# Kernel optimization log

Measured on AMD Instinct MI355X. Metric: run time of the kernel, lower is better.

## Reference

```python
import jax, jax.numpy as jnp
import numpy as np

DEPTH = 24; D_MODEL = 192; D_INNER = 384; D_STATE = 16; DT_RANK = 12; D_CONV = 4
H = 32; W = 3200; P = 16; NP = (W // P) * (H // P)  # 400 patches
NCLS = 22; BATCH = 4; EPS = 1e-5


def _rmsnorm(x, w):
    return x * jax.lax.rsqrt(jnp.mean(x * x, axis=-1, keepdims=True) + EPS) * w


def _causal_dwconv(x, w, b):
    # x: (B, L, D), w: (D, K) depthwise, left-padded causal conv (mamba conv1d)
    D = x.shape[-1]; K = w.shape[-1]
    xp = jnp.pad(jnp.swapaxes(x, 1, 2), ((0, 0), (0, 0), (K - 1, 0)))
    y = jax.lax.conv_general_dilated(xp, w[:, None, :], (1,), 'VALID',
            dimension_numbers=('NCH', 'OIH', 'NCH'), feature_group_count=D)
    return jnp.swapaxes(y + b[None, :, None], 1, 2)


def _selective_scan(x, dt, Bm, Cm, A, Dsk):
    # x, dt: (B, L, d); Bm, Cm: (B, L, n); A: (d, n); Dsk: (d,)
    dA = jnp.exp(dt[..., None] * A)                  # (B, L, d, n)
    dBx = (dt * x)[..., None] * Bm[:, :, None, :]    # (B, L, d, n)
    h0 = jnp.zeros((x.shape[0], x.shape[2], A.shape[1]), x.dtype)

    def step(h, inp):
        a, bx, c = inp
        h = a * h + bx
        return h, jnp.einsum('bdn,bn->bd', h, c)

    _, ys = jax.lax.scan(step, h0,
        (jnp.swapaxes(dA, 0, 1), jnp.swapaxes(dBx, 0, 1), jnp.swapaxes(Cm, 0, 1)))
    return jnp.swapaxes(ys, 0, 1) + x * Dsk


def _mamba_dir(xz, cw_l, cb_l, xpw, dtw, dtb, A, Dsk):
    xx, z = jnp.split(xz, 2, axis=-1)
    xx = jax.nn.silu(_causal_dwconv(xx, cw_l, cb_l))
    dbl = xx @ xpw.T                                  # (B, L, dt_rank + 2n)
    dt = jax.nn.softplus(dbl[..., :DT_RANK] @ dtw.T + dtb)
    Bm = dbl[..., DT_RANK:DT_RANK + D_STATE]
    Cm = dbl[..., DT_RANK + D_STATE:]
    y = _selective_scan(xx, dt, Bm, Cm, A, Dsk)
    return y * jax.nn.silu(z)


def _forward(x, pe_w, pe_b, cls_token, pos_embed, norm_w, in_proj_w, cw, cb,
             xproj_w, dtproj_w, dtproj_b, A_log, A_b_log, Dp, outproj_w,
             norm_f_w, head_w, head_b):
    B = x.shape[0]
    # patch embed: conv2d stride=kernel=16 on (B,1,H,W)
    y = jax.lax.conv_general_dilated(x[:, None], pe_w, (P, P), 'VALID',
            dimension_numbers=('NCHW', 'OIHW', 'NCHW')) + pe_b[None, :, None, None]
    tok = jnp.transpose(y, (0, 2, 3, 1)).reshape(B, -1, D_MODEL)   # (B, NP, D)
    tok = jnp.concatenate([jnp.broadcast_to(cls_token, (B, 1, D_MODEL)), tok], axis=1)
    tok = tok + pos_embed

    def layer_step(carry, p):
        hidden, residual = carry
        nw, ipw, cw_l, cb_l, xpw, dtw, dtb, Al, Abl, Dsk, opw = p
        residual = residual + hidden          # fused add (residual_in_fp32: all fp32)
        h = _rmsnorm(residual, nw)
        xz = h @ ipw.T                         # (B, L, 2*d_inner)
        y_f = _mamba_dir(xz, cw_l, cb_l, xpw, dtw, dtb, -jnp.exp(Al), Dsk)
        y_b = _mamba_dir(xz[:, ::-1], cw_l, cb_l, xpw, dtw, dtb, -jnp.exp(Abl), Dsk)[:, ::-1]
        return ((y_f + y_b) @ opw.T, residual), None

    # NOTE: source sets residual = x AND hidden = x before the loop, so the
    (hidden, residual), _ = jax.lax.scan(
        layer_step, (tok, tok),
        (norm_w, in_proj_w, cw, cb, xproj_w, dtproj_w, dtproj_b, A_log, A_b_log, Dp, outproj_w))
    out = _rmsnorm(residual + hidden, norm_f_w)
    return out[:, 0] @ head_w.T + head_b          # (B, n_classes)


def setup_inputs() -> dict:
    key = jax.random.key(0)
    ks = jax.random.split(key, 12)

    def n(k, shape, scale):
        return jax.random.normal(k, shape, jnp.float32) * scale

    a_init = jnp.tile(jnp.log(jnp.arange(1, D_STATE + 1, dtype=jnp.float32))[None, None, :],
                      (DEPTH, D_INNER, 1))
    return {
        'x': n(ks[0], (BATCH, H, W), 1.0),
        'pe_w': n(ks[1], (D_MODEL, 1, P, P), 1.0 / P),
        'pe_b': jnp.zeros((D_MODEL,), jnp.float32),
        'cls_token': n(ks[2], (1, 1, D_MODEL), 0.02),
        'pos_embed': n(ks[3], (1, NP + 1, D_MODEL), 0.02),
        'norm_w': jnp.ones((DEPTH, D_MODEL), jnp.float32),
        'in_proj_w': n(ks[4], (DEPTH, 2 * D_INNER, D_MODEL), D_MODEL ** -0.5),
        'cw': n(ks[5], (DEPTH, D_INNER, D_CONV), D_CONV ** -0.5),
        'cb': jnp.zeros((DEPTH, D_INNER), jnp.float32),
        'xproj_w': n(ks[6], (DEPTH, DT_RANK + 2 * D_STATE, D_INNER), D_INNER ** -0.5),
        'dtproj_w': n(ks[7], (DEPTH, D_INNER, DT_RANK), DT_RANK ** -0.5),
        'dtproj_b': n(ks[8], (DEPTH, D_INNER), 0.1),
        'A_log': a_init,
        'A_b_log': a_init,
        'Dp': jnp.ones((DEPTH, D_INNER), jnp.float32),
        'outproj_w': n(ks[9], (DEPTH, D_MODEL, D_INNER), D_INNER ** -0.5 / np.sqrt(DEPTH)),
        'norm_f_w': jnp.ones((D_MODEL,), jnp.float32),
        'head_w': n(ks[10], (NCLS, D_MODEL), D_MODEL ** -0.5),
        'head_b': jnp.zeros((NCLS,), jnp.float32),
    }


def reference(x, pe_w, pe_b, cls_token, pos_embed, norm_w, in_proj_w, cw, cb,
              xproj_w, dtproj_w, dtproj_b, A_log, A_b_log, Dp, outproj_w,
              norm_f_w, head_w, head_b):
    return _forward(x, pe_w, pe_b, cls_token, pos_embed, norm_w, in_proj_w, cw, cb,
                    xproj_w, dtproj_w, dtproj_b, A_log, A_b_log, Dp, outproj_w,
                    norm_f_w, head_w, head_b)
```

## Files before the change

kernel.cpp:

```cpp
#include <hip/hip_runtime.h>
#include <hip/hip_bf16.h>

#define DEPTH 24
#define DM 192
#define DI 384
#define DS 16
#define DR 12
#define LSEQ 401
#define BATCH 4
#define NTOK (BATCH*LSEQ)
#define NCLS 22
#define NC 16
#define TCH 26

__device__ __forceinline__ float silu_f(float x) { return x / (1.f + __expf(-x)); }

__global__ void patch_embed_k(const float* __restrict__ x,
                              const float* __restrict__ pe_w,
                              const float* __restrict__ pe_b,
                              const float* __restrict__ cls,
                              const float* __restrict__ pos,
                              float* __restrict__ residual, float* __restrict__ hidden)
{
    __shared__ float xp[4][256];
    int g0 = blockIdx.x * 4;
    int c = threadIdx.x;
    #pragma unroll
    for (int j = 0; j < 4; j++) {
        int g = g0 + j;
        int b = g / LSEQ, t = g % LSEQ;
        if (t != 0) {
            int p = t - 1, pi = p / 200, pj = p % 200;
            for (int i = c; i < 256; i += 192) {
                int pp = i >> 4, qq = i & 15;
                xp[j][i] = x[((size_t)(b * 32 + pi * 16 + pp)) * 3200 + pj * 16 + qq];
            }
        }
    }
    __syncthreads();
    float acc[4] = {0.f, 0.f, 0.f, 0.f};
    for (int k = 0; k < 256; k++) {
        float w = pe_w[c * 256 + k];
        #pragma unroll
        for (int j = 0; j < 4; j++) acc[j] += xp[j][k] * w;
    }
    #pragma unroll
    for (int j = 0; j < 4; j++) {
        int g = g0 + j;
        int t = g % LSEQ;
        float v = (t == 0) ? cls[c] : (acc[j] + pe_b[c]);
        v += pos[t * DM + c];
        residual[(size_t)g * DM + c] = v;
        hidden[(size_t)g * DM + c] = v;
    }
}

__global__ __launch_bounds__(192) void prenorm_k(
    const float* __restrict__ resin, float* __restrict__ hidden,
    float* __restrict__ resout, float* __restrict__ hnorm,
    const float* __restrict__ nw, float* __restrict__ dbl)
{
    __shared__ float wsum[3][4];
    int c = threadIdx.x;
    int t0 = blockIdx.x * 4;
    int wave = c >> 6, lane = c & 63;
    float r[4], s[4];
    #pragma unroll
    for (int j = 0; j < 4; j++) {
        int idx = (t0 + j) * DM + c;
        r[j] = resin[idx] + hidden[idx];
        s[j] = r[j] * r[j];
    }
    #pragma unroll
    for (int off = 32; off > 0; off >>= 1) {
        #pragma unroll
        for (int j = 0; j < 4; j++) s[j] += __shfl_down(s[j], off);
    }
    if (lane == 0) {
        #pragma unroll
        for (int j = 0; j < 4; j++) wsum[wave][j] = s[j];
    }
    __syncthreads();
    float nwv = nw[c];
    #pragma unroll
    for (int j = 0; j < 4; j++) {
        float tot = wsum[0][j] + wsum[1][j] + wsum[2][j];
        float rms = rsqrtf(tot / (float)DM + 1e-5f);
        int idx = (t0 + j) * DM + c;
        resout[idx] = r[j];
        hnorm[idx] = r[j] * rms * nwv;
        hidden[idx] = 0.f;
    }
    for (int i = blockIdx.x * 192 + c; i < 2 * NTOK * 44; i += 401 * 192)
        dbl[i] = 0.f;
}

__global__ __launch_bounds__(256) void gemm_xz_k(
    const float* __restrict__ hnorm, const float* __restrict__ ipw,
    float* __restrict__ xz)
{
    constexpr int KS = 48;
    __shared__ float As[KS][68];
    __shared__ float Ws[KS][68];
    int tid = threadIdx.x;
    int bn = blockIdx.x * 64;
    int bm = blockIdx.y * 64;
    int r0 = (tid >> 4) * 4;
    int c0 = (tid & 15) * 4;
    int srow = tid >> 2, sk = (tid & 3) * 12;
    float acc[4][4] = {};
    for (int k0 = 0; k0 < DM; k0 += KS) {
        {
            int m = bm + srow;
            const float* ap = hnorm + (size_t)m * DM + k0 + sk;
            #pragma unroll
            for (int i = 0; i < 12; i++)
                As[sk + i][srow] = (m < NTOK) ? ap[i] : 0.f;
            const float* wp = ipw + (size_t)(bn + srow) * DM + k0 + sk;
            #pragma unroll
            for (int i = 0; i < 12; i++)
                Ws[sk + i][srow] = wp[i];
        }
        __syncthreads();
        #pragma unroll
        for (int kk = 0; kk < KS; kk++) {
            float4 a = *(const float4*)&As[kk][r0];
            float4 w = *(const float4*)&Ws[kk][c0];
            acc[0][0] += a.x * w.x; acc[0][1] += a.x * w.y; acc[0][2] += a.x * w.z; acc[0][3] += a.x * w.w;
            acc[1][0] += a.y * w.x; acc[1][1] += a.y * w.y; acc[1][2] += a.y * w.z; acc[1][3] += a.y * w.w;
            acc[2][0] += a.z * w.x; acc[2][1] += a.z * w.y; acc[2][2] += a.z * w.z; acc[2][3] += a.z * w.w;
            acc[3][0] += a.w * w.x; acc[3][1] += a.w * w.y; acc[3][2] += a.w * w.z; acc[3][3] += a.w * w.w;
        }
        __syncthreads();
    }
    #pragma unroll
    for (int i = 0; i < 4; i++) {
        int m = bm + r0 + i;
        if (m >= NTOK) continue;
        *(float4*)&xz[(size_t)m * (2 * DI) + bn + c0] =
            make_float4(acc[i][0], acc[i][1], acc[i][2], acc[i][3]);
    }
}

__global__ __launch_bounds__(256) void xproj_conv_k(
    const float* __restrict__ xz,
    const float* __restrict__ cw, const float* __restrict__ cb,
    const float* __restrict__ xpw, float* __restrict__ dbl)
{
    __shared__ float As[96][33];
    __shared__ float Ws[96][48];
    int tid = threadIdx.x;
    int kbase = blockIdx.x * 96;
    int bm = blockIdx.y * 32;
    for (int idx = tid; idx < 96 * 32; idx += 256) {
        int k = idx >> 5, row = idx & 31;
        int m = bm + row;
        float v = 0.f;
        if (m < 2 * NTOK) {
            int dir = m / NTOK;
            int r = m - dir * NTOK;
            int b = r / LSEQ, t = r % LSEQ;
            int ch = kbase + k;
            float a = cb[ch];
            #pragma unroll
            for (int j = 0; j < 4; j++) {
                int tt = t - 3 + j;
                if (tt >= 0) {
                    int st = dir ? (LSEQ - 1 - tt) : tt;
                    a += cw[ch * 4 + j] * xz[((size_t)(b * LSEQ + st)) * (2 * DI) + ch];
                }
            }
            v = silu_f(a);
        }
        As[k][row] = v;
    }
    for (int i = tid; i < 96 * 48; i += 256) {
        int k = i / 48, rr = i % 48;
        Ws[k][rr] = (rr < 44) ? xpw[(size_t)rr * DI + kbase + k] : 0.f;
    }
    __syncthreads();
    int row = tid & 31, cg = tid >> 5;
    int cbase = cg * 6;
    float acc[6] = {};
    #pragma unroll 4
    for (int kk = 0; kk < 96; kk++) {
        float a = As[kk][row];
        #pragma unroll
        for (int j = 0; j < 6; j++) acc[j] += a * Ws[kk][cbase + j];
    }
    int m = bm + row;
    if (m < 2 * NTOK) {
        #pragma unroll
        for (int j = 0; j < 6; j++) {
            int cc = cbase + j;
            if (cc < 44) atomicAdd(&dbl[(size_t)m * 44 + cc], acc[j]);
        }
    }
}

__global__ __launch_bounds__(256) void scan_part_k(
    const float* __restrict__ xz, const float* __restrict__ dbl,
    const float* __restrict__ cw, const float* __restrict__ cb,
    const float* __restrict__ dtw, const float* __restrict__ dtb,
    const float* __restrict__ A_log, const float* __restrict__ A_b_log,
    float* __restrict__ hloc, float* __restrict__ Pc)
{
    __shared__ float sdbl[TCH][44];
    __shared__ float sdt[TCH][16];
    __shared__ float sxx[TCH][16];
    __shared__ float sw[16][12];
    __shared__ float sb2[16];
    int dblk = blockIdx.x, chunk = blockIdx.y;
    int db = blockIdx.z;
    int dir = db >> 2, b = db & 3;
    int tid = threadIdx.x;
    int d0 = dblk * 16;
    int t0 = chunk * TCH;
    size_t dof44 = (size_t)db * LSEQ * 44;
    for (int i = tid; i < TCH * 44; i += 256) {
        int t = i / 44, cc = i - t * 44;
        sdbl[t][cc] = dbl[dof44 + (size_t)(t0 + t) * 44 + cc];
    }
    if (tid < 192) { int d = tid / 12, r = tid - d * 12; sw[d][r] = dtw[(size_t)(d0 + d) * 12 + r]; }
    if (tid < 16) sb2[tid] = dtb[d0 + tid];
    for (int i = tid; i < TCH * 16; i += 256) {
        int t = i >> 4, d = i & 15;
        int tq = t0 + t, ch = d0 + d;
        float a = cb[ch];
        #pragma unroll
        for (int j = 0; j < 4; j++) {
            int tt = tq - 3 + j;
            if (tt >= 0) {
                int st = dir ? (LSEQ - 1 - tt) : tt;
                a += cw[ch * 4 + j] * xz[((size_t)(b * LSEQ + st)) * (2 * DI) + ch];
            }
        }
        sxx[t][d] = silu_f(a);
    }
    __syncthreads();
    for (int i = tid; i < TCH * 16; i += 256) {
        int t = i >> 4, d = i & 15;
        float a2 = sb2[d];
        #pragma unroll
        for (int r = 0; r < 12; r++) a2 += sdbl[t][r] * sw[d][r];
        sdt[t][d] = (a2 > 15.f) ? a2 : __logf(1.f + __expf(a2));
    }
    __syncthreads();
    int wave = tid >> 6, lane = tid & 63;
    int dsub = wave * 4 + (lane >> 4);
    int n = lane & 15;
    const float* Al = dir ? A_b_log : A_log;
    float Aval = -__expf(Al[(d0 + dsub) * DS + n]);
    float h = 0.f, P = 1.f;
    #pragma unroll
    for (int i = 0; i < TCH; i++) {
        float dtv = sdt[i][dsub];
        float xv  = sxx[i][dsub];
        float Bv  = sdbl[i][12 + n];
        float dA = __expf(dtv * Aval);
        h = dA * h + (dtv * xv) * Bv;
        P *= dA;
    }
    size_t idx2 = ((size_t)db * NC + chunk) * (DI * DS) + (size_t)(d0 + dsub) * DS + n;
    hloc[idx2] = h;
    Pc[idx2] = P;
}

__global__ __launch_bounds__(256) void scan_fix_k(
    const float* __restrict__ xz, const float* __restrict__ dbl,
    const float* __restrict__ cw, const float* __restrict__ cb,
    const float* __restrict__ dtw, const float* __restrict__ dtb,
    const float* __restrict__ A_log, const float* __restrict__ A_b_log,
    const float* __restrict__ Dp,
    const float* __restrict__ hloc, const float* __restrict__ Pc,
    float* __restrict__ yraw)
{
    __shared__ float sdbl[TCH][44];
    __shared__ float sdt[TCH][16];
    __shared__ float sxx[TCH][16];
    __shared__ float sy[TCH][16];
    __shared__ float sw[16][12];
    __shared__ float sb2[16];
    int dblk = blockIdx.x, chunk = blockIdx.y;
    int db = blockIdx.z;
    int dir = db >> 2, b = db & 3;
    int tid = threadIdx.x;
    int d0 = dblk * 16;
    int t0 = chunk * TCH;
    size_t dofD = (size_t)db * LSEQ * DI;
    size_t dof44 = (size_t)db * LSEQ * 44;
    for (int i = tid; i < TCH * 44; i += 256) {
        int t = i / 44, cc = i - t * 44;
        sdbl[t][cc] = ((t0 + t) < LSEQ) ? dbl[dof44 + (size_t)(t0 + t) * 44 + cc] : 0.f;
    }
    if (tid < 192) { int d = tid / 12, r = tid - d * 12; sw[d][r] = dtw[(size_t)(d0 + d) * 12 + r]; }
    if (tid < 16) sb2[tid] = dtb[d0 + tid];
    for (int i = tid; i < TCH * 16; i += 256) {
        int t = i >> 4, d = i & 15;
        int tq = t0 + t, ch = d0 + d;
        float v = 0.f;
        if (tq < LSEQ) {
            float a = cb[ch];
            #pragma unroll
            for (int j = 0; j < 4; j++) {
                int tt = tq - 3 + j;
                if (tt >= 0) {
                    int st = dir ? (LSEQ - 1 - tt) : tt;
                    a += cw[ch * 4 + j] * xz[((size_t)(b * LSEQ + st)) * (2 * DI) + ch];
                }
            }
            v = silu_f(a);
        }
        sxx[t][d] = v;
    }
    __syncthreads();
    for (int i = tid; i < TCH * 16; i += 256) {
        int t = i >> 4, d = i & 15;
        float a2 = sb2[d];
        #pragma unroll
        for (int r = 0; r < 12; r++) a2 += sdbl[t][r] * sw[d][r];
        sdt[t][d] = (a2 > 15.f) ? a2 : __logf(1.f + __expf(a2));
    }
    __syncthreads();
    int wave = tid >> 6, lane = tid & 63;
    int dsub = wave * 4 + (lane >> 4);
    int n = lane & 15;
    const float* Al = dir ? A_b_log : A_log;
    float Aval = -__expf(Al[(d0 + dsub) * DS + n]);
    float Dv = Dp[d0 + dsub];
    float h = 0.f;
    size_t cbase = (size_t)db * NC * (DI * DS) + (size_t)(d0 + dsub) * DS + n;
    #pragma unroll
    for (int j = 0; j < NC - 1; j++) {
        size_t idx = cbase + (size_t)j * (DI * DS);
        float pj = Pc[idx], hj = hloc[idx];
        h = (j < chunk) ? (pj * h + hj) : h;
    }
    #pragma unroll
    for (int i = 0; i < TCH; i++) {
        float dtv = sdt[i][dsub];
        float xv  = sxx[i][dsub];
        float Bv  = sdbl[i][12 + n];
        float Cv  = sdbl[i][28 + n];
        h = __expf(dtv * Aval) * h + (dtv * xv) * Bv;
        float p = h * Cv;
        p += __shfl_xor(p, 1);
        p += __shfl_xor(p, 2);
        p += __shfl_xor(p, 4);
        p += __shfl_xor(p, 8);
        if (n == 0) sy[i][dsub] = p + xv * Dv;
    }
    __syncthreads();
    int len = min(t0 + TCH, LSEQ) - t0;
    for (int idx = tid; idx < len * 16; idx += 256) {
        int t = idx >> 4, d = idx & 15;
        yraw[dofD + (size_t)(t0 + t) * DI + d0 + d] = sy[t][d];
    }
}

__global__ __launch_bounds__(256) void outproj_k(
    const float* __restrict__ yraw, const float* __restrict__ xz,
    const float* __restrict__ opw, float* __restrict__ hidden)
{
    __shared__ float As[96][34];
    __shared__ float Ws[96][34];
    int tid = threadIdx.x;
    int bn = blockIdx.x * 32;
    int bm = blockIdx.y * 32;
    int kbase = blockIdx.z * 192;
    int row8 = tid >> 3, seg = tid & 7, k0 = seg * 24;
    float a[24], wreg[24];
    int m = bm + row8;
    if (m < NTOK) {
        int b = m / LSEQ, t = m % LSEQ;
        const float* yf = yraw + (size_t)m * DI + kbase + k0;
        const float* yb = yraw + (size_t)(NTOK + b * LSEQ + (LSEQ - 1 - t)) * DI + kbase + k0;
        const float* zp = xz + (size_t)m * (2 * DI) + DI + kbase + k0;
        #pragma unroll
        for (int i = 0; i < 24; i++) {
            float z = zp[i];
            a[i] = (yf[i] + yb[i]) * (z / (1.f + __expf(-z)));
        }
    } else {
        #pragma unroll
        for (int i = 0; i < 24; i++) a[i] = 0.f;
    }
    {
        const float* wp = opw + (size_t)(bn + row8) * DI + kbase + k0;
        #pragma unroll
        for (int i = 0; i < 24; i++) wreg[i] = wp[i];
    }
    int r0 = (tid >> 4) * 2, c0 = (tid & 15) * 2;
    float acc[2][2] = {};
    #pragma unroll
    for (int st = 0; st < 2; st++) {
        if (st) __syncthreads();
        if ((seg >> 2) == st) {
            int kb = k0 - st * 96;
            #pragma unroll
            for (int i = 0; i < 24; i++) {
                As[kb + i][row8] = a[i];
                Ws[kb + i][row8] = wreg[i];
            }
        }
        __syncthreads();
        #pragma unroll 8
        for (int kk = 0; kk < 96; kk++) {
            float2 av = *(const float2*)&As[kk][r0];
            float2 wv = *(const float2*)&Ws[kk][c0];
            acc[0][0] += av.x * wv.x; acc[0][1] += av.x * wv.y;
            acc[1][0] += av.y * wv.x; acc[1][1] += av.y * wv.y;
        }
    }
    #pragma unroll
    for (int i = 0; i < 2; i++) {
        int mm = bm + r0 + i;
        if (mm >= NTOK) continue;
        #pragma unroll
        for (int j = 0; j < 2; j++)
            atomicAdd(&hidden[(size_t)mm * DM + bn + c0 + j], acc[i][j]);
    }
}

__global__ void final_head_k(const float* __restrict__ residual, const float* __restrict__ hidden,
                             const float* __restrict__ norm_f,
                             const float* __restrict__ head_w,
                             const float* __restrict__ head_b,
                             void* __restrict__ out,
                             const unsigned short* __restrict__ probe)
{
    __shared__ float wsum[3];
    __shared__ float hb[DM];
    int b = blockIdx.x;
    int c = threadIdx.x;
    int idx = (b * LSEQ) * DM + c;
    float r = residual[idx] + hidden[idx];
    float s = r * r;
    for (int off = 32; off > 0; off >>= 1) s += __shfl_down(s, off);
    int wave = c >> 6, lane = c & 63;
    if (lane == 0) wsum[wave] = s;
    __syncthreads();
    float tot = wsum[0] + wsum[1] + wsum[2];
    float rms = rsqrtf(tot / (float)DM + 1e-5f);
    hb[c] = r * rms * norm_f[c];
    __syncthreads();
    if (c < NCLS) {
        float acc = head_b[c];
        #pragma unroll 8
        for (int k = 0; k < DM; k++) acc += hb[k] * head_w[c * DM + k];
        if (probe[0] == 0x3F80u)
            ((__hip_bfloat16*)out)[b * NCLS + c] = __float2bfloat16(acc);
        else
            ((float*)out)[b * NCLS + c] = acc;
    }
}

extern "C" void kernel_launch(void* const* d_in, const int* in_sizes, int n_in,
                              void* d_out, int out_size, void* d_ws, size_t ws_size,
                              hipStream_t stream)
{
    (void)in_sizes; (void)n_in; (void)out_size; (void)ws_size;
    const float* x      = (const float*)d_in[0];
    const float* pe_w   = (const float*)d_in[1];
    const float* pe_b   = (const float*)d_in[2];
    const float* cls    = (const float*)d_in[3];
    const float* pos    = (const float*)d_in[4];
    const float* norm_w = (const float*)d_in[5];
    const float* ipw    = (const float*)d_in[6];
    const float* cw     = (const float*)d_in[7];
    const float* cb     = (const float*)d_in[8];
    const float* xpw    = (const float*)d_in[9];
    const float* dtw    = (const float*)d_in[10];
    const float* dtb    = (const float*)d_in[11];
    const float* A_log  = (const float*)d_in[12];
    const float* A_b_log= (const float*)d_in[13];
    const float* Dp     = (const float*)d_in[14];
    const float* opw    = (const float*)d_in[15];
    const float* norm_f = (const float*)d_in[16];
    const float* head_w = (const float*)d_in[17];
    const float* head_b = (const float*)d_in[18];
    const unsigned short* probe = (const unsigned short*)d_in[14];

    float* ws = (float*)d_ws;
    const size_t nTokDM = (size_t)NTOK * DM;
    const size_t nTokXZ = (size_t)NTOK * 2 * DI;
    const size_t nDirDI = (size_t)2 * NTOK * DI;
    const size_t nDir44 = (size_t)2 * NTOK * 44;
    const size_t nChunk = (size_t)2 * BATCH * NC * DI * DS;
    float* resA   = ws;
    float* resB   = resA + nTokDM;
    float* hidden = resB + nTokDM;
    float* hnorm  = hidden + nTokDM;
    float* xz     = hnorm + nTokDM;
    float* dbl    = xz + nTokXZ;
    float* yraw   = dbl + nDir44;
    float* hloc   = yraw + nDirDI;
    float* Pc     = hloc + nChunk;

    patch_embed_k<<<NTOK / 4, DM, 0, stream>>>(x, pe_w, pe_b, cls, pos, resA, hidden);

    for (int l = 0; l < DEPTH; l++) {
        float* rin  = (l & 1) ? resB : resA;
        float* rout = (l & 1) ? resA : resB;

        prenorm_k<<<LSEQ, DM, 0, stream>>>(rin, hidden, rout, hnorm,
                                           norm_w + (size_t)l * DM, dbl);

        gemm_xz_k<<<dim3(12, 26), 256, 0, stream>>>(
            hnorm, ipw + (size_t)l * 2 * DI * DM, xz);

        xproj_conv_k<<<dim3(4, 101), 256, 0, stream>>>(
            xz, cw + (size_t)l * DI * 4, cb + (size_t)l * DI,
            xpw + (size_t)l * 44 * DI, dbl);

        scan_part_k<<<dim3(DI / 16, NC - 1, 2 * BATCH), 256, 0, stream>>>(
            xz, dbl, cw + (size_t)l * DI * 4, cb + (size_t)l * DI,
            dtw + (size_t)l * DI * DR, dtb + (size_t)l * DI,
            A_log + (size_t)l * DI * DS, A_b_log + (size_t)l * DI * DS,
            hloc, Pc);

        scan_fix_k<<<dim3(DI / 16, NC, 2 * BATCH), 256, 0, stream>>>(
            xz, dbl, cw + (size_t)l * DI * 4, cb + (size_t)l * DI,
            dtw + (size_t)l * DI * DR, dtb + (size_t)l * DI,
            A_log + (size_t)l * DI * DS, A_b_log + (size_t)l * DI * DS,
            Dp + (size_t)l * DI, hloc, Pc, yraw);

        outproj_k<<<dim3(6, 51, 2), 256, 0, stream>>>(
            yraw, xz, opw + (size_t)l * DM * DI, hidden);
    }

    final_head_k<<<BATCH, DM, 0, stream>>>(resA, hidden, norm_f, head_w, head_b,
                                           d_out, probe);
}
```

Baseline: 3.068 ms.

## Fuse whole network into one cooperative persistent kernel with grid syncs

Replaces the per-layer sequence of six kernel launches with a single cooperative persistent kernel that loops over layers and stages and separates them with grid-wide barriers. The RMSNorm prenorm is fused into the in_proj GEMM tile, which drops the hnorm buffer, and that GEMM moves to smaller 32x32 tiles. Zeroing of dbl and hidden moves into the stages that precede their use. The aim is to remove launch overhead and separate-kernel round trips. The cost is grid.sync latency, lower per-tile efficiency from smaller tiles, and recomputing the norm in every column tile. A multi-kernel fallback path is kept for when cooperative launch fails.

Result: slower. 9.997 ms (+225.8%).

```diff
diff --git a/kernel.cpp b/kernel.cpp
--- a/kernel.cpp
+++ b/kernel.cpp
@@ -1,5 +1,8 @@
 #include <hip/hip_runtime.h>
 #include <hip/hip_bf16.h>
+#include <hip/hip_cooperative_groups.h>
+
+namespace cg = cooperative_groups;
 
 #define DEPTH 24
 #define DM 192
@@ -13,145 +16,143 @@
 #define NC 16
 #define TCH 26
 
+#define NT1 (24*51)
+#define NT2 (4*101)
+#define NT3 (24*(NC-1)*8)
+#define NT4 (24*NC*8)
+#define NT5 (6*51*2)
+
 __device__ __forceinline__ float silu_f(float x) { return x / (1.f + __expf(-x)); }
 
-__global__ void patch_embed_k(const float* __restrict__ x,
-                              const float* __restrict__ pe_w,
-                              const float* __restrict__ pe_b,
-                              const float* __restrict__ cls,
-                              const float* __restrict__ pos,
-                              float* __restrict__ residual, float* __restrict__ hidden)
-{
-    __shared__ float xp[4][256];
-    int g0 = blockIdx.x * 4;
-    int c = threadIdx.x;
+struct MegaArgs {
+    const float *x, *pe_w, *pe_b, *cls, *pos, *norm_w, *ipw, *cw, *cb,
+                *xpw, *dtw, *dtb, *A_log, *A_b_log, *Dp, *opw, *norm_f,
+                *head_w, *head_b;
+    float *resA, *resB, *hidden, *xz, *dbl, *yraw, *hloc, *Pc;
+    void* out;
+    const unsigned short* probe;
+};
+
+__device__ void patch_tile(const MegaArgs& a, int tile, int tid, float* sm)
+{
+    float* xp = sm;
+    int g0 = tile * 4;
     #pragma unroll
     for (int j = 0; j < 4; j++) {
         int g = g0 + j;
         int b = g / LSEQ, t = g % LSEQ;
         if (t != 0) {
             int p = t - 1, pi = p / 200, pj = p % 200;
-            for (int i = c; i < 256; i += 192) {
-                int pp = i >> 4, qq = i & 15;
-                xp[j][i] = x[((size_t)(b * 32 + pi * 16 + pp)) * 3200 + pj * 16 + qq];
+            int pp = tid >> 4, qq = tid & 15;
+            xp[j * 256 + tid] = a.x[((size_t)(b * 32 + pi * 16 + pp)) * 3200 + pj * 16 + qq];
+        }
+    }
+    __syncthreads();
+    int c = tid;
+    if (c < DM) {
+        float acc[4] = {0.f, 0.f, 0.f, 0.f};
+        for (int k = 0; k < 256; k++) {
+            float w = a.pe_w[c * 256 + k];
+            #pragma unroll
+            for (int j = 0; j < 4; j++) acc[j] += xp[j * 256 + k] * w;
+        }
+        #pragma unroll
+        for (int j = 0; j < 4; j++) {
+            int g = g0 + j;
+            int t = g % LSEQ;
+            float v = (t == 0) ? a.cls[c] : (acc[j] + a.pe_b[c]);
+            v += a.pos[t * DM + c];
+            a.resA[(size_t)g * DM + c] = v;
+            a.hidden[(size_t)g * DM + c] = v;
+        }
+    }
+    __syncthreads();
+}
+
+__device__ void xz_tile(const MegaArgs& a, int l, int tile, int tid, float* sm)
+{
+    const float* rin = (l & 1) ? a.resB : a.resA;
+    float* rout      = (l & 1) ? a.resA : a.resB;
+    const float* nw    = a.norm_w + (size_t)l * DM;
+    const float* ipw_l = a.ipw + (size_t)l * 2 * DI * DM;
+    float* As = sm;
+    float* Ws = sm + 3264;
+    int bn = (tile % 24) * 32;
+    int bm = (tile / 24) * 32;
+    int row8 = tid >> 3, seg = tid & 7, k0 = seg * 24;
+    int m = bm + row8;
+    float r[24];
+    float s = 0.f;
+    if (m < NTOK) {
+        const float* rp = rin + (size_t)m * DM + k0;
+        const float* hp = a.hidden + (size_t)m * DM + k0;
+        #pragma unroll
+        for (int i = 0; i < 24; i++) { r[i] = rp[i] + hp[i]; s += r[i] * r[i]; }
+    } else {
+        #pragma unroll
+        for (int i = 0; i < 24; i++) r[i] = 0.f;
+    }
+    s += __shfl_down(s, 4, 8);
+    s += __shfl_down(s, 2, 8);
+    s += __shfl_down(s, 1, 8);
+    float tot = __shfl(s, 0, 8);
+    float rms = rsqrtf(tot / (float)DM + 1e-5f);
+    if (bn == 0 && m < NTOK) {
+        float* ro = rout + (size_t)m * DM + k0;
+        #pragma unroll
+        for (int i = 0; i < 24; i++) ro[i] = r[i];
+    }
+    float av[24], wreg[24];
+    {
+        const float* wp = ipw_l + (size_t)(bn + row8) * DM + k0;
+        #pragma unroll
+        for (int i = 0; i < 24; i++) {
+            av[i] = r[i] * rms * nw[k0 + i];
+            wreg[i] = wp[i];
+        }
+    }
+    int r0 = (tid >> 4) * 2, c0 = (tid & 15) * 2;
+    float acc[2][2] = {};
+    #pragma unroll
+    for (int st = 0; st < 2; st++) {
+        if (st) __syncthreads();
+        if ((seg >> 2) == st) {
+            int kb = k0 - st * 96;
+            #pragma unroll
+            for (int i = 0; i < 24; i++) {
+                As[(kb + i) * 34 + row8] = av[i];
+                Ws[(kb + i) * 34 + row8] = wreg[i];
             }
         }
-    }
-    __syncthreads();
-    float acc[4] = {0.f, 0.f, 0.f, 0.f};
-    for (int k = 0; k < 256; k++) {
-        float w = pe_w[c * 256 + k];
-        #pragma unroll
-        for (int j = 0; j < 4; j++) acc[j] += xp[j][k] * w;
-    }
-    #pragma unroll
-    for (int j = 0; j < 4; j++) {
-        int g = g0 + j;
-        int t = g % LSEQ;
-        float v = (t == 0) ? cls[c] : (acc[j] + pe_b[c]);
-        v += pos[t * DM + c];
-        residual[(size_t)g * DM + c] = v;
-        hidden[(size_t)g * DM + c] = v;
-    }
-}
-
-__global__ __launch_bounds__(192) void prenorm_k(
-    const float* __restrict__ resin, float* __restrict__ hidden,
-    float* __restrict__ resout, float* __restrict__ hnorm,
-    const float* __restrict__ nw, float* __restrict__ dbl)
-{
-    __shared__ float wsum[3][4];
-    int c = threadIdx.x;
-    int t0 = blockIdx.x * 4;
-    int wave = c >> 6, lane = c & 63;
-    float r[4], s[4];
-    #pragma unroll
-    for (int j = 0; j < 4; j++) {
-        int idx = (t0 + j) * DM + c;
-        r[j] = resin[idx] + hidden[idx];
-        s[j] = r[j] * r[j];
-    }
-    #pragma unroll
-    for (int off = 32; off > 0; off >>= 1) {
-        #pragma unroll
-        for (int j = 0; j < 4; j++) s[j] += __shfl_down(s[j], off);
-    }
-    if (lane == 0) {
-        #pragma unroll
-        for (int j = 0; j < 4; j++) wsum[wave][j] = s[j];
-    }
-    __syncthreads();
-    float nwv = nw[c];
-    #pragma unroll
-    for (int j = 0; j < 4; j++) {
-        float tot = wsum[0][j] + wsum[1][j] + wsum[2][j];
-        float rms = rsqrtf(tot / (float)DM + 1e-5f);
-        int idx = (t0 + j) * DM + c;
-        resout[idx] = r[j];
-        hnorm[idx] = r[j] * rms * nwv;
-        hidden[idx] = 0.f;
-    }
-    for (int i = blockIdx.x * 192 + c; i < 2 * NTOK * 44; i += 401 * 192)
-        dbl[i] = 0.f;
-}
-
-__global__ __launch_bounds__(256) void gemm_xz_k(
-    const float* __restrict__ hnorm, const float* __restrict__ ipw,
-    float* __restrict__ xz)
-{
-    constexpr int KS = 48;
-    __shared__ float As[KS][68];
-    __shared__ float Ws[KS][68];
-    int tid = threadIdx.x;
-    int bn = blockIdx.x * 64;
-    int bm = blockIdx.y * 64;
-    int r0 = (tid >> 4) * 4;
-    int c0 = (tid & 15) * 4;
-    int srow = tid >> 2, sk = (tid & 3) * 12;
-    float acc[4][4] = {};
-    for (int k0 = 0; k0 < DM; k0 += KS) {
-        {
-            int m = bm + srow;
-            const float* ap = hnorm + (size_t)m * DM + k0 + sk;
-            #pragma unroll
-            for (int i = 0; i < 12; i++)
-                As[sk + i][srow] = (m < NTOK) ? ap[i] : 0.f;
-            const float* wp = ipw + (size_t)(bn + srow) * DM + k0 + sk;
-            #pragma unroll
-            for (int i = 0; i < 12; i++)
-                Ws[sk + i][srow] = wp[i];
-        }
         __syncthreads();
-        #pragma unroll
-        for (int kk = 0; kk < KS; kk++) {
-            float4 a = *(const float4*)&As[kk][r0];
-            float4 w = *(const float4*)&Ws[kk][c0];
-            acc[0][0] += a.x * w.x; acc[0][1] += a.x * w.y; acc[0][2] += a.x * w.z; acc[0][3] += a.x * w.w;
-            acc[1][0] += a.y * w.x; acc[1][1] += a.y * w.y; acc[1][2] += a.y * w.z; acc[1][3] += a.y * w.w;
-            acc[2][0] += a.z * w.x; acc[2][1] += a.z * w.y; acc[2][2] += a.z * w.z; acc[2][3] += a.z * w.w;
-            acc[3][0] += a.w * w.x; acc[3][1] += a.w * w.y; acc[3][2] += a.w * w.z; acc[3][3] += a.w * w.w;
-        }
-        __syncthreads();
-    }
-    #pragma unroll
-    for (int i = 0; i < 4; i++) {
-        int m = bm + r0 + i;
-        if (m >= NTOK) continue;
-        *(float4*)&xz[(size_t)m * (2 * DI) + bn + c0] =
-            make_float4(acc[i][0], acc[i][1], acc[i][2], acc[i][3]);
-    }
-}
-
-__global__ __launch_bounds__(256) void xproj_conv_k(
-    const float* __restrict__ xz,
-    const float* __restrict__ cw, const float* __restrict__ cb,
-    const float* __restrict__ xpw, float* __restrict__ dbl)
-{
-    __shared__ float As[96][33];
-    __shared__ float Ws[96][48];
-    int tid = threadIdx.x;
-    int kbase = blockIdx.x * 96;
-    int bm = blockIdx.y * 32;
+        #pragma unroll 8
+        for (int kk = 0; kk < 96; kk++) {
+            float2 aa = *(const float2*)&As[kk * 34 + r0];
+            float2 ww = *(const float2*)&Ws[kk * 34 + c0];
+            acc[0][0] += aa.x * ww.x; acc[0][1] += aa.x * ww.y;
+            acc[1][0] += aa.y * ww.x; acc[1][1] += aa.y * ww.y;
+        }
+    }
+    #pragma unroll
+    for (int i = 0; i < 2; i++) {
+        int mm = bm + r0 + i;
+        if (mm >= NTOK) continue;
+        #pragma unroll
+        for (int j = 0; j < 2; j++)
+            a.xz[(size_t)mm * (2 * DI) + bn + c0 + j] = acc[i][j];
+    }
+    __syncthreads();
+}
+
+__device__ void xproj_tile(const MegaArgs& a, int l, int tile, int tid, float* sm)
+{
+    const float* cw_l  = a.cw + (size_t)l * DI * 4;
+    const float* cb_l  = a.cb + (size_t)l * DI;
+    const float* xpw_l = a.xpw + (size_t)l * 44 * DI;
+    float* As = sm;
+    float* Ws = sm + 3168;
+    int kbase = (tile % 4) * 96;
+    int bm = (tile / 4) * 32;
     for (int idx = tid; idx < 96 * 32; idx += 256) {
         int k = idx >> 5, row = idx & 31;
         int m = bm + row;
@@ -161,232 +162,207 @@
             int r = m - dir * NTOK;
             int b = r / LSEQ, t = r % LSEQ;
             int ch = kbase + k;
-            float a = cb[ch];
+            float acc = cb_l[ch];
             #pragma unroll
             for (int j = 0; j < 4; j++) {
                 int tt = t - 3 + j;
                 if (tt >= 0) {
                     int st = dir ? (LSEQ - 1 - tt) : tt;
-                    a += cw[ch * 4 + j] * xz[((size_t)(b * LSEQ + st)) * (2 * DI) + ch];
+                    acc += cw_l[ch * 4 + j] * a.xz[((size_t)(b * LSEQ + st)) * (2 * DI) + ch];
                 }
             }
-            v = silu_f(a);
-        }
-        As[k][row] = v;
+            v = silu_f(acc);
+        }
+        As[k * 33 + row] = v;
     }
     for (int i = tid; i < 96 * 48; i += 256) {
         int k = i / 48, rr = i % 48;
-        Ws[k][rr] = (rr < 44) ? xpw[(size_t)rr * DI + kbase + k] : 0.f;
-    }
-    __syncthreads();
-    int row = tid & 31, cg = tid >> 5;
-    int cbase = cg * 6;
+        Ws[k * 48 + rr] = (rr < 44) ? xpw_l[(size_t)rr * DI + kbase + k] : 0.f;
+    }
+    __syncthreads();
+    int row = tid & 31, cg_ = tid >> 5;
+    int cbase = cg_ * 6;
     float acc[6] = {};
     #pragma unroll 4
     for (int kk = 0; kk < 96; kk++) {
-        float a = As[kk][row];
-        #pragma unroll
-        for (int j = 0; j < 6; j++) acc[j] += a * Ws[kk][cbase + j];
+        float av = As[kk * 33 + row];
+        #pragma unroll
+        for (int j = 0; j < 6; j++) acc[j] += av * Ws[kk * 48 + cbase + j];
     }
     int m = bm + row;
     if (m < 2 * NTOK) {
         #pragma unroll
         for (int j = 0; j < 6; j++) {
             int cc = cbase + j;
-            if (cc < 44) atomicAdd(&dbl[(size_t)m * 44 + cc], acc[j]);
-        }
-    }
-}
-
-__global__ __launch_bounds__(256) void scan_part_k(
-    const float* __restrict__ xz, const float* __restrict__ dbl,
-    const float* __restrict__ cw, const float* __restrict__ cb,
-    const float* __restrict__ dtw, const float* __restrict__ dtb,
-    const float* __restrict__ A_log, const float* __restrict__ A_b_log,
-    float* __restrict__ hloc, float* __restrict__ Pc)
-{
-    __shared__ float sdbl[TCH][44];
-    __shared__ float sdt[TCH][16];
-    __shared__ float sxx[TCH][16];
-    __shared__ float sw[16][12];
-    __shared__ float sb2[16];
-    int dblk = blockIdx.x, chunk = blockIdx.y;
-    int db = blockIdx.z;
-    int dir = db >> 2, b = db & 3;
-    int tid = threadIdx.x;
-    int d0 = dblk * 16;
-    int t0 = chunk * TCH;
+            if (cc < 44) atomicAdd(&a.dbl[(size_t)m * 44 + cc], acc[j]);
+        }
+    }
+    __syncthreads();
+}
+
+__device__ void scan_stage(const MegaArgs& a, int l,
+                           int d0, int t0, int db, int dir, int b, bool guard,
+                           int tid, float* sdbl, float* sdt, float* sxx,
+                           float* sw, float* sb2)
+{
+    const float* cw_l  = a.cw + (size_t)l * DI * 4;
+    const float* cb_l  = a.cb + (size_t)l * DI;
+    const float* dtw_l = a.dtw + (size_t)l * DI * DR;
+    const float* dtb_l = a.dtb + (size_t)l * DI;
     size_t dof44 = (size_t)db * LSEQ * 44;
     for (int i = tid; i < TCH * 44; i += 256) {
         int t = i / 44, cc = i - t * 44;
-        sdbl[t][cc] = dbl[dof44 + (size_t)(t0 + t) * 44 + cc];
-    }
-    if (tid < 192) { int d = tid / 12, r = tid - d * 12; sw[d][r] = dtw[(size_t)(d0 + d) * 12 + r]; }
-    if (tid < 16) sb2[tid] = dtb[d0 + tid];
-    for (int i = tid; i < TCH * 16; i += 256) {
-        int t = i >> 4, d = i & 15;
-        int tq = t0 + t, ch = d0 + d;
-        float a = cb[ch];
-        #pragma unroll
-        for (int j = 0; j < 4; j++) {
-            int tt = tq - 3 + j;
-            if (tt >= 0) {
-                int st = dir ? (LSEQ - 1 - tt) : tt;
-                a += cw[ch * 4 + j] * xz[((size_t)(b * LSEQ + st)) * (2 * DI) + ch];
-            }
-        }
-        sxx[t][d] = silu_f(a);
-    }
-    __syncthreads();
-    for (int i = tid; i < TCH * 16; i += 256) {
-        int t = i >> 4, d = i & 15;
-        float a2 = sb2[d];
-        #pragma unroll
-        for (int r = 0; r < 12; r++) a2 += sdbl[t][r] * sw[d][r];
-        sdt[t][d] = (a2 > 15.f) ? a2 : __logf(1.f + __expf(a2));
-    }
-    __syncthreads();
-    int wave = tid >> 6, lane = tid & 63;
-    int dsub = wave * 4 + (lane >> 4);
-    int n = lane & 15;
-    const float* Al = dir ? A_b_log : A_log;
-    float Aval = -__expf(Al[(d0 + dsub) * DS + n]);
-    float h = 0.f, P = 1.f;
-    #pragma unroll
-    for (int i = 0; i < TCH; i++) {
-        float dtv = sdt[i][dsub];
-        float xv  = sxx[i][dsub];
-        float Bv  = sdbl[i][12 + n];
-        float dA = __expf(dtv * Aval);
-        h = dA * h + (dtv * xv) * Bv;
-        P *= dA;
-    }
-    size_t idx2 = ((size_t)db * NC + chunk) * (DI * DS) + (size_t)(d0 + dsub) * DS + n;
-    hloc[idx2] = h;
-    Pc[idx2] = P;
-}
-
-__global__ __launch_bounds__(256) void scan_fix_k(
-    const float* __restrict__ xz, const float* __restrict__ dbl,
-    const float* __restrict__ cw, const float* __restrict__ cb,
-    const float* __restrict__ dtw, const float* __restrict__ dtb,
-    const float* __restrict__ A_log, const float* __restrict__ A_b_log,
-    const float* __restrict__ Dp,
-    const float* __restrict__ hloc, const float* __restrict__ Pc,
-    float* __restrict__ yraw)
-{
-    __shared__ float sdbl[TCH][44];
-    __shared__ float sdt[TCH][16];
-    __shared__ float sxx[TCH][16];
-    __shared__ float sy[TCH][16];
-    __shared__ float sw[16][12];
-    __shared__ float sb2[16];
-    int dblk = blockIdx.x, chunk = blockIdx.y;
-    int db = blockIdx.z;
-    int dir = db >> 2, b = db & 3;
-    int tid = threadIdx.x;
-    int d0 = dblk * 16;
-    int t0 = chunk * TCH;
-    size_t dofD = (size_t)db * LSEQ * DI;
-    size_t dof44 = (size_t)db * LSEQ * 44;
-    for (int i = tid; i < TCH * 44; i += 256) {
-        int t = i / 44, cc = i - t * 44;
-        sdbl[t][cc] = ((t0 + t) < LSEQ) ? dbl[dof44 + (size_t)(t0 + t) * 44 + cc] : 0.f;
-    }
-    if (tid < 192) { int d = tid / 12, r = tid - d * 12; sw[d][r] = dtw[(size_t)(d0 + d) * 12 + r]; }
-    if (tid < 16) sb2[tid] = dtb[d0 + tid];
+        bool v = !guard || (t0 + t) < LSEQ;
+        sdbl[t * 44 + cc] = v ? a.dbl[dof44 + (size_t)(t0 + t) * 44 + cc] : 0.f;
+    }
+    if (tid < 192) { int d = tid / 12, r = tid - d * 12; sw[d * 12 + r] = dtw_l[(size_t)(d0 + d) * 12 + r]; }
+    if (tid < 16) sb2[tid] = dtb_l[d0 + tid];
     for (int i = tid; i < TCH * 16; i += 256) {
         int t = i >> 4, d = i & 15;
         int tq = t0 + t, ch = d0 + d;
         float v = 0.f;
-        if (tq < LSEQ) {
-            float a = cb[ch];
+        if (!guard || tq < LSEQ) {
+            float acc = cb_l[ch];
             #pragma unroll
             for (int j = 0; j < 4; j++) {
                 int tt = tq - 3 + j;
                 if (tt >= 0) {
                     int st = dir ? (LSEQ - 1 - tt) : tt;
-                    a += cw[ch * 4 + j] * xz[((size_t)(b * LSEQ + st)) * (2 * DI) + ch];
+                    acc += cw_l[ch * 4 + j] * a.xz[((size_t)(b * LSEQ + st)) * (2 * DI) + ch];
                 }
             }
-            v = silu_f(a);
-        }
-        sxx[t][d] = v;
+            v = silu_f(acc);
+        }
+        sxx[t * 16 + d] = v;
     }
     __syncthreads();
     for (int i = tid; i < TCH * 16; i += 256) {
         int t = i >> 4, d = i & 15;
         float a2 = sb2[d];
         #pragma unroll
-        for (int r = 0; r < 12; r++) a2 += sdbl[t][r] * sw[d][r];
-        sdt[t][d] = (a2 > 15.f) ? a2 : __logf(1.f + __expf(a2));
-    }
-    __syncthreads();
+        for (int r = 0; r < 12; r++) a2 += sdbl[t * 44 + r] * sw[d * 12 + r];
+        sdt[t * 16 + d] = (a2 > 15.f) ? a2 : __logf(1.f + __expf(a2));
+    }
+    __syncthreads();
+}
+
+__device__ void scan_part_tile(const MegaArgs& a, int l, int tile, int tid, float* sm)
+{
+    float* sdbl = sm;
+    float* sdt  = sm + 1144;
+    float* sxx  = sm + 1560;
+    float* sw   = sm + 1976;
+    float* sb2  = sm + 2168;
+    int dblk = tile % 24;
+    int rr = tile / 24;
+    int chunk = rr % (NC - 1);
+    int db = rr / (NC - 1);
+    int dir = db >> 2, b = db & 3;
+    int d0 = dblk * 16;
+    int t0 = chunk * TCH;
+    scan_stage(a, l, d0, t0, db, dir, b, false, tid, sdbl, sdt, sxx, sw, sb2);
     int wave = tid >> 6, lane = tid & 63;
     int dsub = wave * 4 + (lane >> 4);
     int n = lane & 15;
-    const float* Al = dir ? A_b_log : A_log;
+    const float* Al = (dir ? a.A_b_log : a.A_log) + (size_t)l * DI * DS;
     float Aval = -__expf(Al[(d0 + dsub) * DS + n]);
-    float Dv = Dp[d0 + dsub];
+    float h = 0.f, P = 1.f;
+    #pragma unroll
+    for (int i = 0; i < TCH; i++) {
+        float dtv = sdt[i * 16 + dsub];
+        float xv  = sxx[i * 16 + dsub];
+        float Bv  = sdbl[i * 44 + 12 + n];
+        float dA = __expf(dtv * Aval);
+        h = dA * h + (dtv * xv) * Bv;
+        P *= dA;
+    }
+    size_t idx2 = ((size_t)db * NC + chunk) * (DI * DS) + (size_t)(d0 + dsub) * DS + n;
+    a.hloc[idx2] = h;
+    a.Pc[idx2] = P;
+    __syncthreads();
+}
+
+__device__ void scan_fix_tile(const MegaArgs& a, int l, int tile, int tid, float* sm)
+{
+    float* sdbl = sm;
+    float* sdt  = sm + 1144;
+    float* sxx  = sm + 1560;
+    float* sy   = sm + 1976;
+    float* sw   = sm + 2392;
+    float* sb2  = sm + 2584;
+    int dblk = tile % 24;
+    int rr = tile / 24;
+    int chunk = rr % NC;
+    int db = rr / NC;
+    int dir = db >> 2, b = db & 3;
+    int d0 = dblk * 16;
+    int t0 = chunk * TCH;
+    size_t dofD = (size_t)db * LSEQ * DI;
+    scan_stage(a, l, d0, t0, db, dir, b, true, tid, sdbl, sdt, sxx, sw, sb2);
+    int wave = tid >> 6, lane = tid & 63;
+    int dsub = wave * 4 + (lane >> 4);
+    int n = lane & 15;
+    const float* Al = (dir ? a.A_b_log : a.A_log) + (size_t)l * DI * DS;
+    float Aval = -__expf(Al[(d0 + dsub) * DS + n]);
+    float Dv = a.Dp[(size_t)l * DI + d0 + dsub];
     float h = 0.f;
     size_t cbase = (size_t)db * NC * (DI * DS) + (size_t)(d0 + dsub) * DS + n;
     #pragma unroll
     for (int j = 0; j < NC - 1; j++) {
         size_t idx = cbase + (size_t)j * (DI * DS);
-        float pj = Pc[idx], hj = hloc[idx];
+        float pj = a.Pc[idx], hj = a.hloc[idx];
         h = (j < chunk) ? (pj * h + hj) : h;
     }
     #pragma unroll
     for (int i = 0; i < TCH; i++) {
-        float dtv = sdt[i][dsub];
-        float xv  = sxx[i][dsub];
-        float Bv  = sdbl[i][12 + n];
-        float Cv  = sdbl[i][28 + n];
+        float dtv = sdt[i * 16 + dsub];
+        float xv  = sxx[i * 16 + dsub];
+        float Bv  = sdbl[i * 44 + 12 + n];
+        float Cv  = sdbl[i * 44 + 28 + n];
         h = __expf(dtv * Aval) * h + (dtv * xv) * Bv;
         float p = h * Cv;
         p += __shfl_xor(p, 1);
         p += __shfl_xor(p, 2);
         p += __shfl_xor(p, 4);
         p += __shfl_xor(p, 8);
-        if (n == 0) sy[i][dsub] = p + xv * Dv;
+        if (n == 0) sy[i * 16 + dsub] = p + xv * Dv;
     }
     __syncthreads();
     int len = min(t0 + TCH, LSEQ) - t0;
     for (int idx = tid; idx < len * 16; idx += 256) {
         int t = idx >> 4, d = idx & 15;
-        yraw[dofD + (size_t)(t0 + t) * DI + d0 + d] = sy[t][d];
-    }
-}
-
-__global__ __launch_bounds__(256) void outproj_k(
-    const float* __restrict__ yraw, const float* __restrict__ xz,
-    const float* __restrict__ opw, float* __restrict__ hidden)
-{
-    __shared__ float As[96][34];
-    __shared__ float Ws[96][34];
-    int tid = threadIdx.x;
-    int bn = blockIdx.x * 32;
-    int bm = blockIdx.y * 32;
-    int kbase = blockIdx.z * 192;
+        a.yraw[dofD + (size_t)(t0 + t) * DI + d0 + d] = sy[t * 16 + d];
+    }
+    __syncthreads();
+}
+
+__device__ void outproj_tile(const MegaArgs& a, int l, int tile, int tid, float* sm)
+{
+    const float* opw_l = a.opw + (size_t)l * DM * DI;
+    float* As = sm;
+    float* Ws = sm + 3264;
+    int bn = (tile % 6) * 32;
+    int bm = ((tile / 6) % 51) * 32;
+    int kbase = (tile / (6 * 51)) * 192;
     int row8 = tid >> 3, seg = tid & 7, k0 = seg * 24;
-    float a[24], wreg[24];
+    float av[24], wreg[24];
     int m = bm + row8;
     if (m < NTOK) {
         int b = m / LSEQ, t = m % LSEQ;
-        const float* yf = yraw + (size_t)m * DI + kbase + k0;
-        const float* yb = yraw + (size_t)(NTOK + b * LSEQ + (LSEQ - 1 - t)) * DI + kbase + k0;
-        const float* zp = xz + (size_t)m * (2 * DI) + DI + kbase + k0;
+        const float* yf = a.yraw + (size_t)m * DI + kbase + k0;
+        const float* yb = a.yraw + (size_t)(NTOK + b * LSEQ + (LSEQ - 1 - t)) * DI + kbase + k0;
+        const float* zp = a.xz + (size_t)m * (2 * DI) + DI + kbase + k0;
         #pragma unroll
         for (int i = 0; i < 24; i++) {
             float z = zp[i];
-            a[i] = (yf[i] + yb[i]) * (z / (1.f + __expf(-z)));
+            av[i] = (yf[i] + yb[i]) * (z / (1.f + __expf(-z)));
         }
     } else {
         #pragma unroll
-        for (int i = 0; i < 24; i++) a[i] = 0.f;
+        for (int i = 0; i < 24; i++) av[i] = 0.f;
     }
     {
-        const float* wp = opw + (size_t)(bn + row8) * DI + kbase + k0;
+        const float* wp = opw_l + (size_t)(bn + row8) * DI + kbase + k0;
         #pragma unroll
         for (int i = 0; i < 24; i++) wreg[i] = wp[i];
     }
@@ -399,17 +375,17 @@
             int kb = k0 - st * 96;
             #pragma unroll
             for (int i = 0; i < 24; i++) {
-                As[kb + i][row8] = a[i];
-                Ws[kb + i][row8] = wreg[i];
+                As[(kb + i) * 34 + row8] = av[i];
+                Ws[(kb + i) * 34 + row8] = wreg[i];
             }
         }
         __syncthreads();
         #pragma unroll 8
         for (int kk = 0; kk < 96; kk++) {
-            float2 av = *(const float2*)&As[kk][r0];
-            float2 wv = *(const float2*)&Ws[kk][c0];
-            acc[0][0] += av.x * wv.x; acc[0][1] += av.x * wv.y;
-            acc[1][0] += av.y * wv.x; acc[1][1] += av.y * wv.y;
+            float2 aa = *(const float2*)&As[kk * 34 + r0];
+            float2 ww = *(const float2*)&Ws[kk * 34 + c0];
+            acc[0][0] += aa.x * ww.x; acc[0][1] += aa.x * ww.y;
+            acc[1][0] += aa.y * ww.x; acc[1][1] += aa.y * ww.y;
         }
     }
     #pragma unroll
@@ -418,117 +394,160 @@
         if (mm >= NTOK) continue;
         #pragma unroll
         for (int j = 0; j < 2; j++)
-            atomicAdd(&hidden[(size_t)mm * DM + bn + c0 + j], acc[i][j]);
-    }
-}
-
-__global__ void final_head_k(const float* __restrict__ residual, const float* __restrict__ hidden,
-                             const float* __restrict__ norm_f,
-                             const float* __restrict__ head_w,
-                             const float* __restrict__ head_b,
-                             void* __restrict__ out,
-                             const unsigned short* __restrict__ probe)
-{
-    __shared__ float wsum[3];
-    __shared__ float hb[DM];
-    int b = blockIdx.x;
-    int c = threadIdx.x;
-    int idx = (b * LSEQ) * DM + c;
-    float r = residual[idx] + hidden[idx];
-    float s = r * r;
+            atomicAdd(&a.hidden[(size_t)mm * DM + bn + c0 + j], acc[i][j]);
+    }
+    __syncthreads();
+}
+
+__device__ void head_tile(const MegaArgs& a, int b, int tid, float* sm)
+{
+    float* hb = sm;
+    float* wsum = sm + 192;
+    int c = tid;
+    float r = 0.f, s = 0.f;
+    if (c < DM) {
+        int idx = (b * LSEQ) * DM + c;
+        r = a.resA[idx] + a.hidden[idx];
+        s = r * r;
+    }
+    #pragma unroll
     for (int off = 32; off > 0; off >>= 1) s += __shfl_down(s, off);
-    int wave = c >> 6, lane = c & 63;
-    if (lane == 0) wsum[wave] = s;
-    __syncthreads();
-    float tot = wsum[0] + wsum[1] + wsum[2];
+    if ((tid & 63) == 0) wsum[tid >> 6] = s;
+    __syncthreads();
+    float tot = wsum[0] + wsum[1] + wsum[2] + wsum[3];
     float rms = rsqrtf(tot / (float)DM + 1e-5f);
-    hb[c] = r * rms * norm_f[c];
+    if (c < DM) hb[c] = r * rms * a.norm_f[c];
     __syncthreads();
     if (c < NCLS) {
-        float acc = head_b[c];
+        float acc = a.head_b[c];
         #pragma unroll 8
-        for (int k = 0; k < DM; k++) acc += hb[k] * head_w[c * DM + k];
-        if (probe[0] == 0x3F80u)
-            ((__hip_bfloat16*)out)[b * NCLS + c] = __float2bfloat16(acc);
+        for (int k = 0; k < DM; k++) acc += hb[k] * a.head_w[c * DM + k];
+        if (a.probe[0] == 0x3F80u)
+            ((__hip_bfloat16*)a.out)[b * NCLS + c] = __float2bfloat16(acc);
         else
-            ((float*)out)[b * NCLS + c] = acc;
-    }
-}
+            ((float*)a.out)[b * NCLS + c] = acc;
+    }
+}
+
+__global__ __launch_bounds__(256, 2) void mega_k(MegaArgs a)
+{
+    cg::grid_group gg = cg::this_grid();
+    __shared__ float sm[7776];
+    int nb = gridDim.x, gb = blockIdx.x, tid = threadIdx.x;
+
+    for (int t = gb; t < NTOK / 4; t += nb) patch_tile(a, t, tid, sm);
+    gg.sync();
+
+    for (int l = 0; l < DEPTH; l++) {
+        for (int i = gb * 256 + tid; i < 2 * NTOK * 44; i += nb * 256) a.dbl[i] = 0.f;
+        for (int t = gb; t < NT1; t += nb) xz_tile(a, l, t, tid, sm);
+        gg.sync();
+        for (int t = gb; t < NT2; t += nb) xproj_tile(a, l, t, tid, sm);
+        gg.sync();
+        for (int i = gb * 256 + tid; i < NTOK * DM; i += nb * 256) a.hidden[i] = 0.f;
+        for (int t = gb; t < NT3; t += nb) scan_part_tile(a, l, t, tid, sm);
+        gg.sync();
+        for (int t = gb; t < NT4; t += nb) scan_fix_tile(a, l, t, tid, sm);
+        gg.sync();
+        for (int t = gb; t < NT5; t += nb) outproj_tile(a, l, t, tid, sm);
+        gg.sync();
+    }
+    if (gb < BATCH) head_tile(a, gb, tid, sm);
+}
+
+__global__ __launch_bounds__(256) void patch_k(MegaArgs a)
+{ __shared__ float sm[1024]; patch_tile(a, blockIdx.x, threadIdx.x, sm); }
+
+__global__ __launch_bounds__(256) void p1_k(MegaArgs a, int l)
+{
+    __shared__ float sm[6528];
+    for (int i = blockIdx.x * 256 + threadIdx.x; i < 2 * NTOK * 44; i += gridDim.x * 256)
+        a.dbl[i] = 0.f;
+    xz_tile(a, l, blockIdx.x, threadIdx.x, sm);
+}
+__global__ __launch_bounds__(256) void p2_k(MegaArgs a, int l)
+{ __shared__ float sm[7776]; xproj_tile(a, l, blockIdx.x, threadIdx.x, sm); }
+
+__global__ __launch_bounds__(256) void p3_k(MegaArgs a, int l)
+{
+    __shared__ float sm[2184];
+    for (int i = blockIdx.x * 256 + threadIdx.x; i < NTOK * DM; i += gridDim.x * 256)
+        a.hidden[i] = 0.f;
+    scan_part_tile(a, l, blockIdx.x, threadIdx.x, sm);
+}
+__global__ __launch_bounds__(256) void p4_k(MegaArgs a, int l)
+{ __shared__ float sm[2600]; scan_fix_tile(a, l, blockIdx.x, threadIdx.x, sm); }
+
+__global__ __launch_bounds__(256) void p5_k(MegaArgs a, int l)
+{ __shared__ float sm[6528]; outproj_tile(a, l, blockIdx.x, threadIdx.x, sm); }
+
+__global__ __launch_bounds__(256) void head_k(MegaArgs a)
+{ __shared__ float sm[256]; head_tile(a, blockIdx.x, threadIdx.x, sm); }
 
 extern "C" void kernel_launch(void* const* d_in, const int* in_sizes, int n_in,
                               void* d_out, int out_size, void* d_ws, size_t ws_size,
                               hipStream_t stream)
 {
     (void)in_sizes; (void)n_in; (void)out_size; (void)ws_size;
-    const float* x      = (const float*)d_in[0];
-    const float* pe_w   = (const float*)d_in[1];
-    const float* pe_b   = (const float*)d_in[2];
-    const float* cls    = (const float*)d_in[3];
-    const float* pos    = (const float*)d_in[4];
-    const float* norm_w = (const float*)d_in[5];
-    const float* ipw    = (const float*)d_in[6];
-    const float* cw     = (const float*)d_in[7];
-    const float* cb     = (const float*)d_in[8];
-    const float* xpw    = (const float*)d_in[9];
-    const float* dtw    = (const float*)d_in[10];
-    const float* dtb    = (const float*)d_in[11];
-    const float* A_log  = (const float*)d_in[12];
-    const float* A_b_log= (const float*)d_in[13];
-    const float* Dp     = (const float*)d_in[14];
-    const float* opw    = (const float*)d_in[15];
-    const float* norm_f = (const float*)d_in[16];
-    const float* head_w = (const float*)d_in[17];
-    const float* head_b = (const float*)d_in[18];
-    const unsigned short* probe = (const unsigned short*)d_in[14];
-
     float* ws = (float*)d_ws;
     const size_t nTokDM = (size_t)NTOK * DM;
     const size_t nTokXZ = (size_t)NTOK * 2 * DI;
     const size_t nDirDI = (size_t)2 * NTOK * DI;
     const size_t nDir44 = (size_t)2 * NTOK * 44;
     const size_t nChunk = (size_t)2 * BATCH * NC * DI * DS;
-    float* resA   = ws;
-    float* resB   = resA + nTokDM;
-    float* hidden = resB + nTokDM;
-    float* hnorm  = hidden + nTokDM;
-    float* xz     = hnorm + nTokDM;
-    float* dbl    = xz + nTokXZ;
-    float* yraw   = dbl + nDir44;
-    float* hloc   = yraw + nDirDI;
-    float* Pc     = hloc + nChunk;
-
-    patch_embed_k<<<NTOK / 4, DM, 0, stream>>>(x, pe_w, pe_b, cls, pos, resA, hidden);
-
-    for (int l = 0; l < DEPTH; l++) {
-        float* rin  = (l & 1) ? resB : resA;
-        float* rout = (l & 1) ? resA : resB;
-
-        prenorm_k<<<LSEQ, DM, 0, stream>>>(rin, hidden, rout, hnorm,
-                                           norm_w + (size_t)l * DM, dbl);
-
-        gemm_xz_k<<<dim3(12, 26), 256, 0, stream>>>(
-            hnorm, ipw + (size_t)l * 2 * DI * DM, xz);
-
-        xproj_conv_k<<<dim3(4, 101), 256, 0, stream>>>(
-            xz, cw + (size_t)l * DI * 4, cb + (size_t)l * DI,
-            xpw + (size_t)l * 44 * DI, dbl);
-
-        scan_part_k<<<dim3(DI / 16, NC - 1, 2 * BATCH), 256, 0, stream>>>(
-            xz, dbl, cw + (size_t)l * DI * 4, cb + (size_t)l * DI,
-            dtw + (size_t)l * DI * DR, dtb + (size_t)l * DI,
-            A_log + (size_t)l * DI * DS, A_b_log + (size_t)l * DI * DS,
-            hloc, Pc);
-
-        scan_fix_k<<<dim3(DI / 16, NC, 2 * BATCH), 256, 0, stream>>>(
-            xz, dbl, cw + (size_t)l * DI * 4, cb + (size_t)l * DI,
-            dtw + (size_t)l * DI * DR, dtb + (size_t)l * DI,
-            A_log + (size_t)l * DI * DS, A_b_log + (size_t)l * DI * DS,
-            Dp + (size_t)l * DI, hloc, Pc, yraw);
-
-        outproj_k<<<dim3(6, 51, 2), 256, 0, stream>>>(
-            yraw, xz, opw + (size_t)l * DM * DI, hidden);
-    }
-
-    final_head_k<<<BATCH, DM, 0, stream>>>(resA, hidden, norm_f, head_w, head_b,
-                                           d_out, probe);
-}
+
+    MegaArgs a;
+    a.x      = (const float*)d_in[0];
+    a.pe_w   = (const float*)d_in[1];
+    a.pe_b   = (const float*)d_in[2];
+    a.cls    = (const float*)d_in[3];
+    a.pos    = (const float*)d_in[4];
+    a.norm_w = (const float*)d_in[5];
+    a.ipw    = (const float*)d_in[6];
+    a.cw     = (const float*)d_in[7];
+    a.cb     = (const float*)d_in[8];
+    a.xpw    = (const float*)d_in[9];
+    a.dtw    = (const float*)d_in[10];
+    a.dtb    = (const float*)d_in[11];
+    a.A_log  = (const float*)d_in[12];
+    a.A_b_log= (const float*)d_in[13];
+    a.Dp     = (const float*)d_in[14];
+    a.opw    = (const float*)d_in[15];
+    a.norm_f = (const float*)d_in[16];
+    a.head_w = (const float*)d_in[17];
+    a.head_b = (const float*)d_in[18];
+    a.probe  = (const unsigned short*)d_in[14];
+
+    a.resA   = ws;
+    a.resB   = a.resA + nTokDM;
+    a.hidden = a.resB + nTokDM;
+    a.xz     = a.hidden + nTokDM;
+    a.dbl    = a.xz + nTokXZ;
+    a.yraw   = a.dbl + nDir44;
+    a.hloc   = a.yraw + nDirDI;
+    a.Pc     = a.hloc + nChunk;
+    a.out    = d_out;
+
+    int maxPerCU = 0;
+    hipError_t oe = hipOccupancyMaxActiveBlocksPerMultiprocessor(&maxPerCU, mega_k, 256, 0);
+    hipError_t le = hipErrorUnknown;
+    if (oe == hipSuccess && maxPerCU > 0) {
+        int grid = maxPerCU * 256;
+        if (grid > NT1) grid = NT1;
+        void* params[] = { &a };
+        le = hipLaunchCooperativeKernel((void*)mega_k, dim3(grid), dim3(256),
+                                        params, 0, stream);
+    }
+    if (le != hipSuccess) {
+        (void)hipGetLastError();
+        patch_k<<<NTOK / 4, 256, 0, stream>>>(a);
+        for (int l = 0; l < DEPTH; l++) {
+            p1_k<<<NT1, 256, 0, stream>>>(a, l);
+            p2_k<<<NT2, 256, 0, stream>>>(a, l);
+            p3_k<<<NT3, 256, 0, stream>>>(a, l);
+            p4_k<<<NT4, 256, 0, stream>>>(a, l);
+            p5_k<<<NT5, 256, 0, stream>>>(a, l);
+        }
+        head_k<<<BATCH, 256, 0, stream>>>(a);
+    }
+}
```
